# Optimization experiments

Hardware: AMD Instinct MI355X
Metric: run time of the kernel (lower is better)

The kernel has to match this reference:

```python
import jax, jax.numpy as jnp
import numpy as np

N_A, N_P = 50000, 100000          # author / paper node counts
E_W, E_C = 1600000, 3200000       # writes & written_by edges, cites edges
NEG_SLOPE = 0.2                   # DGL GATConv default leaky_relu slope
EPS = 1e-12                       # F.normalize eps


def _gat(h_src, h_dst, src, dst, W, al, ar, b, n_dst):
    """DGL GATConv: fc -> per-head additive attention -> edge softmax -> weighted sum + bias."""
    H, F = al.shape
    fs = (h_src @ W.T).reshape(-1, H, F)            # [Ns, H, F]
    fd = (h_dst @ W.T).reshape(-1, H, F)            # [Nd, H, F]
    el = (fs * al).sum(-1)                          # [Ns, H]
    er = (fd * ar).sum(-1)                          # [Nd, H]
    e = jax.nn.leaky_relu(el[src] + er[dst], NEG_SLOPE)      # [E, H]
    m = jax.lax.stop_gradient(jax.ops.segment_max(e, dst, num_segments=n_dst))
    ex = jnp.exp(e - m[dst])
    s = jax.ops.segment_sum(ex, dst, num_segments=n_dst)
    a = ex / s[dst]                                 # edge softmax per dst node, per head
    rst = jax.ops.segment_sum(fs[src] * a[:, :, None], dst, num_segments=n_dst)
    return rst + b.reshape(H, F)                    # [Nd, H, F]


def _l2norm(x):
    return x / jnp.maximum(jnp.linalg.norm(x, axis=1, keepdims=True), EPS)


def setup_inputs() -> dict:
    key = jax.random.key(0)
    ks = iter(jax.random.split(key, 64))
    def nrm(shape, scale=0.1):
        return jax.random.normal(next(ks), shape, dtype=jnp.float32) * scale
    inp = {
        'feat_author': jax.random.normal(next(ks), (N_A, 128), dtype=jnp.float32),
        'feat_paper':  jax.random.normal(next(ks), (N_P, 256), dtype=jnp.float32),
        'fm_W_author': nrm((64, 128)), 'fm_b_author': nrm((64,)),
        'fm_W_paper':  nrm((64, 256)), 'fm_b_paper':  nrm((64,)),
    }
    for e in ('writes', 'written_by', 'cites'):
        inp[f'g1_{e}_W'] = nrm((64, 64)); inp[f'g1_{e}_al'] = nrm((4, 16))
        inp[f'g1_{e}_ar'] = nrm((4, 16)); inp[f'g1_{e}_b'] = nrm((64,))
        inp[f'g2_{e}_W'] = nrm((64, 64)); inp[f'g2_{e}_al'] = nrm((1, 64))
        inp[f'g2_{e}_ar'] = nrm((1, 64)); inp[f'g2_{e}_b'] = nrm((64,))
    inp['w_src'] = jax.random.randint(next(ks), (E_W,), 0, N_A, dtype=jnp.int32)
    inp['w_dst'] = jax.random.randint(next(ks), (E_W,), 0, N_P, dtype=jnp.int32)
    inp['wb_src'] = jax.random.randint(next(ks), (E_W,), 0, N_P, dtype=jnp.int32)
    inp['wb_dst'] = jax.random.randint(next(ks), (E_W,), 0, N_A, dtype=jnp.int32)
    inp['c_src'] = jax.random.randint(next(ks), (E_C,), 0, N_P, dtype=jnp.int32)
    inp['c_dst'] = jax.random.randint(next(ks), (E_C,), 0, N_P, dtype=jnp.int32)
    return inp


def reference(feat_author, feat_paper, fm_W_author, fm_b_author, fm_W_paper, fm_b_paper,
              g1_writes_W, g1_writes_al, g1_writes_ar, g1_writes_b,
              g2_writes_W, g2_writes_al, g2_writes_ar, g2_writes_b,
              g1_written_by_W, g1_written_by_al, g1_written_by_ar, g1_written_by_b,
              g2_written_by_W, g2_written_by_al, g2_written_by_ar, g2_written_by_b,
              g1_cites_W, g1_cites_al, g1_cites_ar, g1_cites_b,
              g2_cites_W, g2_cites_al, g2_cites_ar, g2_cites_b,
              w_src, w_dst, wb_src, wb_dst, c_src, c_dst):
    # FeatureMappingLayer: per-ntype Linear -> relu, out_dim 64
    h_a = jax.nn.relu(feat_author @ fm_W_author.T + fm_b_author)
    h_p = jax.nn.relu(feat_paper @ fm_W_paper.T + fm_b_paper)
    # NodeAttentionLayer: per-etype GATConv(64 -> 16, 4 heads), flatten, sum over incoming etypes
    h1_p = (_gat(h_a, h_p, w_src, w_dst, g1_writes_W, g1_writes_al, g1_writes_ar, g1_writes_b, N_P)
            + _gat(h_p, h_p, c_src, c_dst, g1_cites_W, g1_cites_al, g1_cites_ar, g1_cites_b, N_P)
           ).reshape(N_P, 64)
    h1_a = _gat(h_p, h_a, wb_src, wb_dst, g1_written_by_W, g1_written_by_al, g1_written_by_ar,
                g1_written_by_b, N_A).reshape(N_A, 64)
    # gat2: per-etype GATConv(64 -> 64, 1 head) on h1[:, :64] (== h1), squeeze, sum
    h2_p = (_gat(h1_a, h1_p, w_src, w_dst, g2_writes_W, g2_writes_al, g2_writes_ar, g2_writes_b, N_P)
            + _gat(h1_p, h1_p, c_src, c_dst, g2_cites_W, g2_cites_al, g2_cites_ar, g2_cites_b, N_P)
           ).reshape(N_P, 64)
    h2_a = _gat(h1_p, h1_a, wb_src, wb_dst, g2_written_by_W, g2_written_by_al, g2_written_by_ar,
                g2_written_by_b, N_A).reshape(N_A, 64)
    # F.normalize(p=2, dim=1)
    return (_l2norm(h2_a), _l2norm(h2_p))
```

## Files before the change

kernel.cpp:

```cpp
#include <hip/hip_runtime.h>
#include <hip/hip_bf16.h>

#define N_A 50000
#define N_P 100000
#define E_W 1600000
#define E_C 3200000
#define HA (N_A*64)
#define HP (N_P*64)

typedef __attribute__((ext_vector_type(8))) short short8_t;
typedef __attribute__((ext_vector_type(4))) float f32x4;

__device__ __forceinline__ unsigned short f2b(float f)
{
    __hip_bfloat16 b = __float2bfloat16(f);
    return *reinterpret_cast<unsigned short*>(&b);
}

__global__ __launch_bounds__(256) void gemm_fm2(
        const float* __restrict__ X0, const float* __restrict__ W0,
        const float* __restrict__ b0, float* __restrict__ out0, int M0, int K0, int nb0,
        const float* __restrict__ X1, const float* __restrict__ W1,
        const float* __restrict__ b1, float* __restrict__ out1, int M1, int K1)
{
    __shared__ unsigned short Xs[128][72];
    __shared__ unsigned short Wsh[64][72];
    const float *X, *W, *bias; float* out; int M, K, row0;
    if ((int)blockIdx.x < nb0) {
        X = X0; W = W0; bias = b0; out = out0; M = M0; K = K0; row0 = blockIdx.x * 128;
    } else {
        X = X1; W = W1; bias = b1; out = out1; M = M1; K = K1;
        row0 = ((int)blockIdx.x - nb0) * 128;
    }
    int tid = threadIdx.x, lane = tid & 63, wv = tid >> 6;
    int m = lane & 15, kb = lane >> 4;

    f32x4 acc[2][4];
#pragma unroll
    for (int rb = 0; rb < 2; ++rb)
#pragma unroll
        for (int cb = 0; cb < 4; ++cb) acc[rb][cb] = (f32x4){0.f, 0.f, 0.f, 0.f};

    for (int k0 = 0; k0 < K; k0 += 64) {
        int rbase = (tid >> 4) * 8;
        int c4 = (tid & 15) * 4;
#pragma unroll
        for (int i = 0; i < 8; ++i) {
            int rg = row0 + rbase + i; if (rg >= M) rg = M - 1;
            float4 v = *reinterpret_cast<const float4*>(&X[(long)rg * K + k0 + c4]);
            Xs[rbase + i][c4 + 0] = f2b(v.x);
            Xs[rbase + i][c4 + 1] = f2b(v.y);
            Xs[rbase + i][c4 + 2] = f2b(v.z);
            Xs[rbase + i][c4 + 3] = f2b(v.w);
        }
        int wr = tid >> 2;
        int wc = (tid & 3) * 16;
#pragma unroll
        for (int q = 0; q < 4; ++q) {
            float4 v = *reinterpret_cast<const float4*>(&W[(long)wr * K + k0 + wc + q * 4]);
            Wsh[wr][wc + q * 4 + 0] = f2b(v.x);
            Wsh[wr][wc + q * 4 + 1] = f2b(v.y);
            Wsh[wr][wc + q * 4 + 2] = f2b(v.z);
            Wsh[wr][wc + q * 4 + 3] = f2b(v.w);
        }
        __syncthreads();
#pragma unroll
        for (int kc = 0; kc < 2; ++kc) {
            short8_t a0 = *reinterpret_cast<const short8_t*>(&Xs[wv * 32 + m][kc * 32 + kb * 8]);
            short8_t a1 = *reinterpret_cast<const short8_t*>(&Xs[wv * 32 + 16 + m][kc * 32 + kb * 8]);
#pragma unroll
            for (int cb = 0; cb < 4; ++cb) {
                short8_t b = *reinterpret_cast<const short8_t*>(&Wsh[cb * 16 + m][kc * 32 + kb * 8]);
                acc[0][cb] = __builtin_amdgcn_mfma_f32_16x16x32_bf16(a0, b, acc[0][cb], 0, 0, 0);
                acc[1][cb] = __builtin_amdgcn_mfma_f32_16x16x32_bf16(a1, b, acc[1][cb], 0, 0, 0);
            }
        }
        __syncthreads();
    }

#pragma unroll
    for (int rb = 0; rb < 2; ++rb)
#pragma unroll
    for (int j = 0; j < 4; ++j) {
        int r = row0 + wv * 32 + rb * 16 + (lane >> 4) * 4 + j;
        if (r < M) {
#pragma unroll
            for (int cb = 0; cb < 4; ++cb) {
                int c = cb * 16 + m;
                float v = acc[rb][cb][j] + bias[c];
                out[(long)r * 64 + c] = fmaxf(v, 0.f);
            }
        }
    }
}

__global__ __launch_bounds__(256) void proj3(
        const float* __restrict__ X0, const float* __restrict__ W0,
        unsigned short* __restrict__ o0, int M0, int nb0,
        const float* __restrict__ X1, const float* __restrict__ W1,
        unsigned short* __restrict__ o1, int M1, int nb1,
        const float* __restrict__ X2, const float* __restrict__ W2,
        unsigned short* __restrict__ o2, int M2)
{
    __shared__ unsigned short Xs[128][72];
    __shared__ unsigned short Wsh[64][72];
    const float *X, *W; unsigned short* out; int M, row0;
    if ((int)blockIdx.x < nb0) {
        X = X0; W = W0; out = o0; M = M0; row0 = blockIdx.x * 128;
    } else if ((int)blockIdx.x < nb0 + nb1) {
        X = X1; W = W1; out = o1; M = M1; row0 = ((int)blockIdx.x - nb0) * 128;
    } else {
        X = X2; W = W2; out = o2; M = M2; row0 = ((int)blockIdx.x - nb0 - nb1) * 128;
    }
    int tid = threadIdx.x, lane = tid & 63, wv = tid >> 6;
    int m = lane & 15, kb = lane >> 4;

    int rbase = (tid >> 4) * 8;
    int c4 = (tid & 15) * 4;
#pragma unroll
    for (int i = 0; i < 8; ++i) {
        int rg = row0 + rbase + i; if (rg >= M) rg = M - 1;
        float4 v = *reinterpret_cast<const float4*>(&X[(long)rg * 64 + c4]);
        Xs[rbase + i][c4 + 0] = f2b(v.x);
        Xs[rbase + i][c4 + 1] = f2b(v.y);
        Xs[rbase + i][c4 + 2] = f2b(v.z);
        Xs[rbase + i][c4 + 3] = f2b(v.w);
    }
    int wr = tid >> 2;
    int wc = (tid & 3) * 16;
#pragma unroll
    for (int q = 0; q < 4; ++q) {
        float4 v = *reinterpret_cast<const float4*>(&W[(long)wr * 64 + wc + q * 4]);
        Wsh[wr][wc + q * 4 + 0] = f2b(v.x);
        Wsh[wr][wc + q * 4 + 1] = f2b(v.y);
        Wsh[wr][wc + q * 4 + 2] = f2b(v.z);
        Wsh[wr][wc + q * 4 + 3] = f2b(v.w);
    }
    __syncthreads();

    f32x4 acc[2][4];
#pragma unroll
    for (int rb = 0; rb < 2; ++rb)
#pragma unroll
        for (int cb = 0; cb < 4; ++cb) acc[rb][cb] = (f32x4){0.f, 0.f, 0.f, 0.f};
#pragma unroll
    for (int kc = 0; kc < 2; ++kc) {
        short8_t a0 = *reinterpret_cast<const short8_t*>(&Xs[wv * 32 + m][kc * 32 + kb * 8]);
        short8_t a1 = *reinterpret_cast<const short8_t*>(&Xs[wv * 32 + 16 + m][kc * 32 + kb * 8]);
#pragma unroll
        for (int cb = 0; cb < 4; ++cb) {
            short8_t b = *reinterpret_cast<const short8_t*>(&Wsh[cb * 16 + m][kc * 32 + kb * 8]);
            acc[0][cb] = __builtin_amdgcn_mfma_f32_16x16x32_bf16(a0, b, acc[0][cb], 0, 0, 0);
            acc[1][cb] = __builtin_amdgcn_mfma_f32_16x16x32_bf16(a1, b, acc[1][cb], 0, 0, 0);
        }
    }
#pragma unroll
    for (int rb = 0; rb < 2; ++rb)
#pragma unroll
    for (int j = 0; j < 4; ++j) {
        int r = row0 + wv * 32 + rb * 16 + (lane >> 4) * 4 + j;
        if (r < M) {
#pragma unroll
            for (int cb = 0; cb < 4; ++cb)
                out[(long)r * 64 + cb * 16 + m] = f2b(acc[rb][cb][j]);
        }
    }
}

struct PA { const float* W; const float* a; float* o; int H; };
__global__ void prep_attn12(PA p0, PA p1, PA p2, PA p3, PA p4, PA p5,
                            PA p6, PA p7, PA p8, PA p9, PA p10, PA p11)
{
    PA p;
    switch (blockIdx.x) {
        case 0: p = p0; break;  case 1: p = p1; break;  case 2: p = p2; break;
        case 3: p = p3; break;  case 4: p = p4; break;  case 5: p = p5; break;
        case 6: p = p6; break;  case 7: p = p7; break;  case 8: p = p8; break;
        case 9: p = p9; break;  case 10: p = p10; break; default: p = p11; break;
    }
    int k = threadIdx.x;
    int F = 64 / p.H;
    for (int hh = 0; hh < p.H; ++hh) {
        float s = 0.f;
        for (int f = 0; f < F; ++f)
            s = fmaf(p.W[(hh * F + f) * 64 + k], p.a[hh * F + f], s);
        p.o[k * p.H + hh] = s;
    }
}

__global__ __launch_bounds__(256) void attnvec_mat(
        const float* __restrict__ hP, int NPn,
        const float* __restrict__ fP0, float* __restrict__ oP0,
        const float* __restrict__ fP1, float* __restrict__ oP1,
        const float* __restrict__ fP2, float* __restrict__ oP2,
        const float* __restrict__ fP3, float* __restrict__ oP3,
        const float* __restrict__ hA, int NAn,
        const float* __restrict__ fA0, float* __restrict__ oA0,
        const float* __restrict__ fA1, float* __restrict__ oA1,
        int H, int hb)
{
    __shared__ float hs[64 * 66];
    int tid = threadIdx.x;
    int slotsP = (H == 4) ? 16 : 4;
    int npbP = 256 / slotsP;
    int blocksP = (NPn + npbP - 1) / npbP;

    const float* hsrc; int node0, npb, slots, ncols, N;
    const float* fv0; const float* fv1; const float* fv2; const float* fv3;
    float* ov0; float* ov1; float* ov2; float* ov3;
    if ((int)blockIdx.x < blocksP) {
        hsrc = hP; N = NPn; slots = slotsP; npb = npbP;
        node0 = blockIdx.x * npb;
        ncols = 4 * H;
        fv0 = fP0; ov0 = oP0; fv1 = fP1; ov1 = oP1;
        fv2 = fP2; ov2 = oP2; fv3 = fP3; ov3 = oP3;
    } else {
        int b = (int)blockIdx.x - blocksP;
        hsrc = hA; N = NAn;
        slots = (H == 4) ? 8 : 4; npb = 256 / slots;
        node0 = b * npb;
        ncols = 2 * H;
        fv0 = fA0; ov0 = oA0; fv1 = fA1; ov1 = oA1;
        fv2 = fA0; ov2 = oA0; fv3 = fA1; ov3 = oA1;
    }

    for (int idx = tid; idx < npb * 64; idx += 256) {
        int row = idx >> 6, k = idx & 63;
        int g = node0 + row; if (g >= N) g = N - 1;
        hs[row * 66 + k] = hsrc[(long)g * 64 + k];
    }
    __syncthreads();

    int sshift = (slots == 16) ? 4 : (slots == 8) ? 3 : 2;
    int nl = tid >> sshift;
    int c = tid & (slots - 1);
    int node = node0 + nl;
    if (node >= N || c >= ncols || nl >= npb) return;
    int f = c >> hb;
    int hh = c & (H - 1);
    const float* fv = (f == 0) ? fv0 : (f == 1) ? fv1 : (f == 2) ? fv2 : fv3;
    float* ov = (f == 0) ? ov0 : (f == 1) ? ov1 : (f == 2) ? ov2 : ov3;

    float s = 0.f;
    const float* hrow = &hs[nl * 66];
#pragma unroll 8
    for (int k = 0; k < 64; ++k)
        s = fmaf(hrow[k], fv[k * H + hh], s);
    ov[(long)node * H + hh] = s;
}

__global__ void bucket_hist3(const int* __restrict__ d0, int E0, int* __restrict__ b0,
                             const int* __restrict__ d1, int E1, int* __restrict__ b1,
                             const int* __restrict__ d2, int E2, int* __restrict__ b2,
                             int shift, int blocksPer)
{
    int g = blockIdx.x / blocksPer, bb = blockIdx.x - g * blocksPer;
    const int* dst = g == 0 ? d0 : g == 1 ? d1 : d2;
    int E = g == 0 ? E0 : g == 1 ? E1 : E2;
    int* bcnt = g == 0 ? b0 : g == 1 ? b1 : b2;
    __shared__ int h[256];
    int tid = threadIdx.x;
    h[tid] = 0;
    __syncthreads();
    for (long i = (long)bb * 256 + tid; i < E; i += (long)blocksPer * 256)
        atomicAdd(&h[dst[i] >> shift], 1);
    __syncthreads();
    if (h[tid]) atomicAdd(&bcnt[tid], h[tid]);
}

__global__ void bucket_scan3(int* __restrict__ bcnt, int* __restrict__ bstart,
                             int* __restrict__ gcur,
                             int* __restrict__ o0, int Nn0, int Ee0,
                             int* __restrict__ o1, int Nn1, int Ee1,
                             int* __restrict__ o2, int Nn2, int Ee2)
{
    int g = blockIdx.x;
    int* bc = bcnt + g * 256;
    int* bs = bstart + g * 257;
    int* gc = gcur + g * 256;
    int* offs = g == 0 ? o0 : g == 1 ? o1 : o2;
    int N = g == 0 ? Nn0 : g == 1 ? Nn1 : Nn2;
    int E = g == 0 ? Ee0 : g == 1 ? Ee1 : Ee2;
    __shared__ int sc[256];
    int tid = threadIdx.x;
    int v = bc[tid];
    sc[tid] = v;
    __syncthreads();
    for (int off = 1; off < 256; off <<= 1) {
        int t = (tid >= off) ? sc[tid - off] : 0;
        __syncthreads();
        sc[tid] += t;
        __syncthreads();
    }
    int excl = sc[tid] - v;
    bs[tid] = excl;
    gc[tid] = excl;
    if (tid == 255) bs[256] = E;
    if (tid == 0) offs[N] = E;
}

#define EPT 8
__global__ __launch_bounds__(256) void part3(
        const int* __restrict__ s0, const int* __restrict__ d0, int E0, int nb0,
        uint2* __restrict__ p0,
        const int* __restrict__ s1, const int* __restrict__ d1, int E1, int nb1,
        uint2* __restrict__ p1,
        const int* __restrict__ s2g, const int* __restrict__ d2g, int E2,
        uint2* __restrict__ p2,
        int* __restrict__ gcur3, int shift)
{
    const int* src; const int* dst; int E; uint2* pairs; int* gcur; long base;
    if ((int)blockIdx.x < nb0) {
        src = s0; dst = d0; E = E0; pairs = p0; gcur = gcur3;
        base = (long)blockIdx.x * (256 * EPT);
    } else if ((int)blockIdx.x < nb0 + nb1) {
        src = s1; dst = d1; E = E1; pairs = p1; gcur = gcur3 + 256;
        base = (long)((int)blockIdx.x - nb0) * (256 * EPT);
    } else {
        src = s2g; dst = d2g; E = E2; pairs = p2; gcur = gcur3 + 512;
        base = (long)((int)blockIdx.x - nb0 - nb1) * (256 * EPT);
    }
    __shared__ int hcnt[256];
    __shared__ int hbase[256];
    int tid = threadIdx.x;
    hcnt[tid] = 0;
    __syncthreads();
    int b[EPT], r[EPT], s[EPT], d[EPT];
#pragma unroll
    for (int k = 0; k < EPT; ++k) {
        long idx = base + k * 256 + tid;
        if (idx < E) {
            s[k] = src[idx]; d[k] = dst[idx];
            b[k] = d[k] >> shift;
            r[k] = atomicAdd(&hcnt[b[k]], 1);
        } else b[k] = -1;
    }
    __syncthreads();
    if (hcnt[tid]) hbase[tid] = atomicAdd(&gcur[tid], hcnt[tid]);
    __syncthreads();
#pragma unroll
    for (int k = 0; k < EPT; ++k) {
        if (b[k] >= 0)
            pairs[hbase[b[k]] + r[k]] = make_uint2((unsigned)s[k], (unsigned)d[k]);
    }
}

__global__ __launch_bounds__(512) void csr_fin3(
        const uint2* __restrict__ p0, const int* __restrict__ bs0,
        int* __restrict__ of0, int* __restrict__ c0, int N0, int NB0,
        const uint2* __restrict__ p1, const int* __restrict__ bs1,
        int* __restrict__ of1, int* __restrict__ c1, int N1, int NB1,
        const uint2* __restrict__ p2, const int* __restrict__ bs2,
        int* __restrict__ of2, int* __restrict__ c2, int N2,
        int shift)
{
    const uint2* pairs; const int* bstart; int* offs; int* csr; int N, b;
    if ((int)blockIdx.x < NB0) {
        pairs = p0; bstart = bs0; offs = of0; csr = c0; N = N0; b = blockIdx.x;
    } else if ((int)blockIdx.x < NB0 + NB1) {
        pairs = p1; bstart = bs1; offs = of1; csr = c1; N = N1; b = (int)blockIdx.x - NB0;
    } else {
        pairs = p2; bstart = bs2; offs = of2; csr = c2; N = N2;
        b = (int)blockIdx.x - NB0 - NB1;
    }
    __shared__ int cnt[512];
    __shared__ int sc[512];
    int tid = threadIdx.x;
    int d0 = b << shift;
    int pS = bstart[b], pE = bstart[b + 1];
    cnt[tid] = 0;
    __syncthreads();
    for (int i = pS + tid; i < pE; i += 512)
        atomicAdd(&cnt[pairs[i].y - d0], 1);
    __syncthreads();
    int v = cnt[tid];
    sc[tid] = v;
    __syncthreads();
    for (int off = 1; off < 512; off <<= 1) {
        int t = (tid >= off) ? sc[tid - off] : 0;
        __syncthreads();
        sc[tid] += t;
        __syncthreads();
    }
    int excl = sc[tid] - v;
    if (d0 + tid < N) offs[d0 + tid] = pS + excl;
    cnt[tid] = excl;
    __syncthreads();
    for (int i = pS + tid; i < pE; i += 512) {
        uint2 u = pairs[i];
        int p = atomicAdd(&cnt[u.y - d0], 1);
        csr[pS + p] = (int)u.x;
    }
}

__device__ __forceinline__ void gat_graph(int d, const int* __restrict__ offs,
        const int* __restrict__ csr, const float* __restrict__ el,
        const float* __restrict__ er, const unsigned short* __restrict__ P,
        int hshift, int lane, float* o)
{
    int H = 1 << hshift;
    int off = offs[d];
    int n = offs[d + 1] - off;
    if (n == 0) return;
    int g8 = lane >> 3;
    int fo = (lane & 7) * 8;
    int hf = (hshift == 2) ? ((lane & 7) >> 1) : 0;
    int h = lane & (H - 1);
    float erd = er[d * H + h];
    int estep = 64 >> hshift;
    int i0 = lane >> hshift;
    float acc[8];
#pragma unroll
    for (int q = 0; q < 8; ++q) acc[q] = 0.f;
    float ssum = 0.f;

    int sn_c = 0; float elv_c = 0.f;
    if (i0 < n) { sn_c = csr[off + i0]; elv_c = el[sn_c * H + h]; }

    for (int base = 0; base < n; base += estep) {
        int inext = base + estep + i0;
        int sn_n = 0; float elv_n = 0.f;
        if (inext < n) { sn_n = csr[off + inext]; elv_n = el[sn_n * H + h]; }

        float a = 0.f;
        if (base + i0 < n) {
            float v = elv_c + erd;
            v = v > 0.f ? v : 0.2f * v;
            a = __expf(v);
            ssum += a;
        }
        int rounds = min(estep, n - base);
#pragma unroll 2
        for (int r = 0; r * 8 < rounds; ++r) {
            int sl = r * 8 + g8;
            int lsn = sl << hshift;
            int s2 = __shfl(sn_c, lsn, 64);
            float a2 = __shfl(a, lsn | hf, 64);
            uint4 u = *reinterpret_cast<const uint4*>(&P[(long)s2 * 64 + fo]);
            acc[0] = fmaf(__uint_as_float(u.x << 16), a2, acc[0]);
            acc[1] = fmaf(__uint_as_float(u.x & 0xffff0000u), a2, acc[1]);
            acc[2] = fmaf(__uint_as_float(u.y << 16), a2, acc[2]);
            acc[3] = fmaf(__uint_as_float(u.y & 0xffff0000u), a2, acc[3]);
            acc[4] = fmaf(__uint_as_float(u.z << 16), a2, acc[4]);
            acc[5] = fmaf(__uint_as_float(u.z & 0xffff0000u), a2, acc[5]);
            acc[6] = fmaf(__uint_as_float(u.w << 16), a2, acc[6]);
            acc[7] = fmaf(__uint_as_float(u.w & 0xffff0000u), a2, acc[7]);
        }
        sn_c = sn_n; elv_c = elv_n;
    }

    for (int oo = H; oo < 64; oo <<= 1) ssum += __shfl_xor(ssum, oo, 64);
    float rinv = 1.f / __shfl(ssum, hf, 64);
#pragma unroll
    for (int q = 0; q < 8; ++q) {
        acc[q] += __shfl_xor(acc[q], 8, 64);
        acc[q] += __shfl_xor(acc[q], 16, 64);
        acc[q] += __shfl_xor(acc[q], 32, 64);
        o[q] = fmaf(acc[q], rinv, o[q]);
    }
}

__global__ void gat_fused(
        int NPn, const int* __restrict__ w_offs, const int* __restrict__ w_csr,
        const float* __restrict__ el_w, const float* __restrict__ er_w,
        const unsigned short* __restrict__ Pw,
        const int* __restrict__ c_offs, const int* __restrict__ c_csr,
        const float* __restrict__ el_c, const float* __restrict__ er_c,
        const unsigned short* __restrict__ Pc,
        const float* __restrict__ bP0, const float* __restrict__ bP1,
        float* __restrict__ outP,
        int NAn, const int* __restrict__ wb_offs, const int* __restrict__ wb_csr,
        const float* __restrict__ el_wb, const float* __restrict__ er_wb,
        const unsigned short* __restrict__ Pwb,
        const float* __restrict__ bA0, float* __restrict__ outA,
        int hshift, int doNorm)
{
    int blocksP = (NPn + 3) >> 2;
    int lane = threadIdx.x & 63;
    int sub = threadIdx.x >> 6;
    int fo = (lane & 7) * 8;
    float o[8];
    float* dst;

    if ((int)blockIdx.x < blocksP) {
        int d = ((int)blockIdx.x << 2) | sub;
        if (d >= NPn) return;
#pragma unroll
        for (int q = 0; q < 8; ++q) o[q] = bP0[fo + q] + bP1[fo + q];
        gat_graph(d, w_offs, w_csr, el_w, er_w, Pw, hshift, lane, o);
        gat_graph(d, c_offs, c_csr, el_c, er_c, Pc, hshift, lane, o);
        dst = outP + (long)d * 64;
    } else {
        int d = (((int)blockIdx.x - blocksP) << 2) | sub;
        if (d >= NAn) return;
#pragma unroll
        for (int q = 0; q < 8; ++q) o[q] = bA0[fo + q];
        gat_graph(d, wb_offs, wb_csr, el_wb, er_wb, Pwb, hshift, lane, o);
        dst = outA + (long)d * 64;
    }

    if (doNorm) {
        float ss = 0.f;
#pragma unroll
        for (int q = 0; q < 8; ++q) ss = fmaf(o[q], o[q], ss);
        ss += __shfl_xor(ss, 1, 64);
        ss += __shfl_xor(ss, 2, 64);
        ss += __shfl_xor(ss, 4, 64);
        float sc = 1.f / fmaxf(sqrtf(ss), 1e-12f);
#pragma unroll
        for (int q = 0; q < 8; ++q) o[q] *= sc;
    }
    if (lane < 8) {
        float4 o0, o1;
        o0.x = o[0]; o0.y = o[1]; o0.z = o[2]; o0.w = o[3];
        o1.x = o[4]; o1.y = o[5]; o1.z = o[6]; o1.w = o[7];
        *reinterpret_cast<float4*>(dst + fo) = o0;
        *reinterpret_cast<float4*>(dst + fo + 4) = o1;
    }
}

extern "C" void kernel_launch(void* const* d_in, const int* in_sizes, int n_in,
                              void* d_out, int out_size, void* d_ws, size_t ws_size,
                              hipStream_t stream)
{
    const float* feat_a = (const float*)d_in[0];
    const float* feat_p = (const float*)d_in[1];
    const float* fmWa = (const float*)d_in[2];
    const float* fmba = (const float*)d_in[3];
    const float* fmWp = (const float*)d_in[4];
    const float* fmbp = (const float*)d_in[5];
    const float* g1w_W = (const float*)d_in[6];  const float* g1w_al = (const float*)d_in[7];
    const float* g1w_ar = (const float*)d_in[8]; const float* g1w_b = (const float*)d_in[9];
    const float* g2w_W = (const float*)d_in[10]; const float* g2w_al = (const float*)d_in[11];
    const float* g2w_ar = (const float*)d_in[12]; const float* g2w_b = (const float*)d_in[13];
    const float* g1wb_W = (const float*)d_in[14]; const float* g1wb_al = (const float*)d_in[15];
    const float* g1wb_ar = (const float*)d_in[16]; const float* g1wb_b = (const float*)d_in[17];
    const float* g2wb_W = (const float*)d_in[18]; const float* g2wb_al = (const float*)d_in[19];
    const float* g2wb_ar = (const float*)d_in[20]; const float* g2wb_b = (const float*)d_in[21];
    const float* g1c_W = (const float*)d_in[22]; const float* g1c_al = (const float*)d_in[23];
    const float* g1c_ar = (const float*)d_in[24]; const float* g1c_b = (const float*)d_in[25];
    const float* g2c_W = (const float*)d_in[26]; const float* g2c_al = (const float*)d_in[27];
    const float* g2c_ar = (const float*)d_in[28]; const float* g2c_b = (const float*)d_in[29];
    const int* w_src = (const int*)d_in[30];
    const int* w_dst = (const int*)d_in[31];
    const int* wb_src = (const int*)d_in[32];
    const int* wb_dst = (const int*)d_in[33];
    const int* c_src = (const int*)d_in[34];
    const int* c_dst = (const int*)d_in[35];

    float* ws = (float*)d_ws;
    size_t off = 0;
    auto alloc = [&](size_t n) { float* p = ws + off; off += n; return p; };
    float* h_a  = alloc(HA);
    float* h_p  = alloc(HP);
    float* h1_p = alloc(HP);
    float* h1_a = alloc(HA);
    uint2* pairs_w  = (uint2*)h_a;
    uint2* pairs_c  = (uint2*)h_a + E_W;
    uint2* pairs_wb = (uint2*)h_a + E_W + E_C;
    unsigned short* Pw  = (unsigned short*)alloc(HA / 2 + 16);
    unsigned short* Pc  = (unsigned short*)alloc(HP / 2 + 16);
    unsigned short* Pwb = (unsigned short*)alloc(HP / 2 + 16);
    float* el_w  = alloc((size_t)N_A * 4);
    float* er_w  = alloc((size_t)N_P * 4);
    float* el_c  = alloc((size_t)N_P * 4);
    float* er_c  = alloc((size_t)N_P * 4);
    float* el_wb = alloc((size_t)N_P * 4);
    float* er_wb = alloc((size_t)N_A * 4);
    float* fold  = alloc(12 * 256);
    int* w_offs  = (int*)alloc(N_P + 1);
    int* c_offs  = (int*)alloc(N_P + 1);
    int* wb_offs = (int*)alloc(N_A + 1);
    int* bcnt3   = (int*)alloc(3 * 256);
    int* bstart3 = (int*)alloc(3 * 257);
    int* gcur3   = (int*)alloc(3 * 256);
    int* w_csr   = (int*)alloc(E_W);
    int* c_csr   = (int*)alloc(E_C);
    int* wb_csr  = (int*)alloc(E_W);

    float* wal_w1 = fold + 0*256,  *war_w1 = fold + 1*256;
    float* wal_c1 = fold + 2*256,  *war_c1 = fold + 3*256;
    float* wal_b1 = fold + 4*256,  *war_b1 = fold + 5*256;
    float* wal_w2 = fold + 6*256,  *war_w2 = fold + 7*256;
    float* wal_c2 = fold + 8*256,  *war_c2 = fold + 9*256;
    float* wal_b2 = fold + 10*256, *war_b2 = fold + 11*256;

    const int SHIFT = 9;
    int NB_P = (N_P + 511) >> 9;
    int NB_A = (N_A + 511) >> 9;

    hipMemsetAsync(bcnt3, 0, 3 * 256 * sizeof(int), stream);
    bucket_hist3<<<3 * 256, 256, 0, stream>>>(w_dst, E_W, bcnt3,
                                              c_dst, E_C, bcnt3 + 256,
                                              wb_dst, E_W, bcnt3 + 512, SHIFT, 256);
    bucket_scan3<<<3, 256, 0, stream>>>(bcnt3, bstart3, gcur3,
                                        w_offs, N_P, E_W,
                                        c_offs, N_P, E_C,
                                        wb_offs, N_A, E_W);
    {
        int nbW = (E_W + 2047) / 2048, nbC = (E_C + 2047) / 2048;
        part3<<<nbW + nbC + nbW, 256, 0, stream>>>(
            w_src, w_dst, E_W, nbW, pairs_w,
            c_src, c_dst, E_C, nbC, pairs_c,
            wb_src, wb_dst, E_W, pairs_wb, gcur3, SHIFT);
        csr_fin3<<<NB_P + NB_P + NB_A, 512, 0, stream>>>(
            pairs_w, bstart3, w_offs, w_csr, N_P, NB_P,
            pairs_c, bstart3 + 257, c_offs, c_csr, N_P, NB_P,
            pairs_wb, bstart3 + 514, wb_offs, wb_csr, N_A, SHIFT);
    }

    prep_attn12<<<12, 64, 0, stream>>>(
        PA{g1w_W,  g1w_al,  wal_w1, 4}, PA{g1w_W,  g1w_ar,  war_w1, 4},
        PA{g1c_W,  g1c_al,  wal_c1, 4}, PA{g1c_W,  g1c_ar,  war_c1, 4},
        PA{g1wb_W, g1wb_al, wal_b1, 4}, PA{g1wb_W, g1wb_ar, war_b1, 4},
        PA{g2w_W,  g2w_al,  wal_w2, 1}, PA{g2w_W,  g2w_ar,  war_w2, 1},
        PA{g2c_W,  g2c_al,  wal_c2, 1}, PA{g2c_W,  g2c_ar,  war_c2, 1},
        PA{g2wb_W, g2wb_al, wal_b2, 1}, PA{g2wb_W, g2wb_ar, war_b2, 1});

    {
        int nb0 = (N_A + 127) / 128;
        int nb1 = (N_P + 127) / 128;
        gemm_fm2<<<nb0 + nb1, 256, 0, stream>>>(feat_a, fmWa, fmba, h_a, N_A, 128, nb0,
                                                feat_p, fmWp, fmbp, h_p, N_P, 256);
    }

    int nbA = (N_A + 127) / 128, nbP = (N_P + 127) / 128;
    int gatGrid = (N_P + 3) / 4 + (N_A + 3) / 4;

    {
        int npbP = 16, npbA = 32;
        int grid = (N_P + npbP - 1) / npbP + (N_A + npbA - 1) / npbA;
        attnvec_mat<<<grid, 256, 0, stream>>>(
            h_p, N_P, wal_c1, el_c, war_c1, er_c, war_w1, er_w, wal_b1, el_wb,
            h_a, N_A, wal_w1, el_w, war_b1, er_wb, 4, 2);
    }
    proj3<<<nbA + 2 * nbP, 256, 0, stream>>>(h_a, g1w_W, Pw, N_A, nbA,
                                             h_p, g1c_W, Pc, N_P, nbP,
                                             h_p, g1wb_W, Pwb, N_P);
    gat_fused<<<gatGrid, 256, 0, stream>>>(
        N_P, w_offs, w_csr, el_w, er_w, Pw,
        c_offs, c_csr, el_c, er_c, Pc, g1w_b, g1c_b, h1_p,
        N_A, wb_offs, wb_csr, el_wb, er_wb, Pwb, g1wb_b, h1_a, 2, 0);

    {
        int npbP = 64, npbA = 64;
        int grid = (N_P + npbP - 1) / npbP + (N_A + npbA - 1) / npbA;
        attnvec_mat<<<grid, 256, 0, stream>>>(
            h1_p, N_P, wal_c2, el_c, war_c2, er_c, war_w2, er_w, wal_b2, el_wb,
            h1_a, N_A, wal_w2, el_w, war_b2, er_wb, 1, 0);
    }
    proj3<<<nbA + 2 * nbP, 256, 0, stream>>>(h1_a, g2w_W, Pw, N_A, nbA,
                                             h1_p, g2c_W, Pc, N_P, nbP,
                                             h1_p, g2wb_W, Pwb, N_P);
    float* out = (float*)d_out;
    gat_fused<<<gatGrid, 256, 0, stream>>>(
        N_P, w_offs, w_csr, el_w, er_w, Pw,
        c_offs, c_csr, el_c, er_c, Pc, g2w_b, g2c_b, out + HA,
        N_A, wb_offs, wb_csr, el_wb, er_wb, Pwb, g2wb_b, out, 0, 1);
}
```

Before: 735.4 us.

## Fuse attention-logit computation into projection kernel and use nontemporal CSR loads

Removes the separate attnvec_mat kernel and computes the el/er attention logits inside the projection kernel, reusing the bf16 node rows already staged in shared memory. This saves one launch per layer and a second full read of the hidden features. The logits are now computed from bf16-rounded inputs rather than fp32, which slightly changes precision. The CSR index loads in the GAT aggregation are also made nontemporal to reduce cache pollution.

```diff
diff --git a/kernel.cpp b/kernel.cpp
--- a/kernel.cpp
+++ b/kernel.cpp
@@ -15,6 +15,10 @@
 {
     __hip_bfloat16 b = __float2bfloat16(f);
     return *reinterpret_cast<unsigned short*>(&b);
+}
+__device__ __forceinline__ float b2f(unsigned short u)
+{
+    return __uint_as_float((unsigned)u << 16);
 }
 
 __global__ __launch_bounds__(256) void gemm_fm2(
@@ -94,23 +98,35 @@
     }
 }
 
-__global__ __launch_bounds__(256) void proj3(
+__global__ __launch_bounds__(256) void proj3a(
         const float* __restrict__ X0, const float* __restrict__ W0,
         unsigned short* __restrict__ o0, int M0, int nb0,
+        const float* __restrict__ fA0, float* __restrict__ eA0,
+        const float* __restrict__ fA1, float* __restrict__ eA1,
         const float* __restrict__ X1, const float* __restrict__ W1,
         unsigned short* __restrict__ o1, int M1, int nb1,
+        const float* __restrict__ fP0, float* __restrict__ eP0,
+        const float* __restrict__ fP1, float* __restrict__ eP1,
+        const float* __restrict__ fP2, float* __restrict__ eP2,
+        const float* __restrict__ fP3, float* __restrict__ eP3,
         const float* __restrict__ X2, const float* __restrict__ W2,
-        unsigned short* __restrict__ o2, int M2)
+        unsigned short* __restrict__ o2, int M2, int H)
 {
     __shared__ unsigned short Xs[128][72];
     __shared__ unsigned short Wsh[64][72];
-    const float *X, *W; unsigned short* out; int M, row0;
+    const float *X, *W; unsigned short* out; int M, row0, nf;
+    const float* fv[4]; float* ev[4];
     if ((int)blockIdx.x < nb0) {
         X = X0; W = W0; out = o0; M = M0; row0 = blockIdx.x * 128;
+        nf = 2; fv[0] = fA0; ev[0] = eA0; fv[1] = fA1; ev[1] = eA1;
+        fv[2] = fA0; ev[2] = eA0; fv[3] = fA1; ev[3] = eA1;
     } else if ((int)blockIdx.x < nb0 + nb1) {
         X = X1; W = W1; out = o1; M = M1; row0 = ((int)blockIdx.x - nb0) * 128;
+        nf = 4; fv[0] = fP0; ev[0] = eP0; fv[1] = fP1; ev[1] = eP1;
+        fv[2] = fP2; ev[2] = eP2; fv[3] = fP3; ev[3] = eP3;
     } else {
         X = X2; W = W2; out = o2; M = M2; row0 = ((int)blockIdx.x - nb0 - nb1) * 128;
+        nf = 0;
     }
     int tid = threadIdx.x, lane = tid & 63, wv = tid >> 6;
     int m = lane & 15, kb = lane >> 4;
@@ -165,6 +181,25 @@
                 out[(long)r * 64 + cb * 16 + m] = f2b(acc[rb][cb][j]);
         }
     }
+
+    if (nf) {
+        int tot = 128 * nf * H;
+        for (int t = tid; t < tot; t += 256) {
+            int row = t / (nf * H);
+            int rest = t - row * (nf * H);
+            int f = rest / H;
+            int hh = rest - f * H;
+            int r = row0 + row;
+            if (r >= M) continue;
+            const unsigned short* xr = Xs[row];
+            const float* fvv = fv[f];
+            float s = 0.f;
+#pragma unroll 8
+            for (int k = 0; k < 64; ++k)
+                s = fmaf(b2f(xr[k]), fvv[k * H + hh], s);
+            ev[f][(long)r * H + hh] = s;
+        }
+    }
 }
 
 struct PA { const float* W; const float* a; float* o; int H; };
@@ -186,67 +221,6 @@
             s = fmaf(p.W[(hh * F + f) * 64 + k], p.a[hh * F + f], s);
         p.o[k * p.H + hh] = s;
     }
-}
-
-__global__ __launch_bounds__(256) void attnvec_mat(
-        const float* __restrict__ hP, int NPn,
-        const float* __restrict__ fP0, float* __restrict__ oP0,
-        const float* __restrict__ fP1, float* __restrict__ oP1,
-        const float* __restrict__ fP2, float* __restrict__ oP2,
-        const float* __restrict__ fP3, float* __restrict__ oP3,
-        const float* __restrict__ hA, int NAn,
-        const float* __restrict__ fA0, float* __restrict__ oA0,
-        const float* __restrict__ fA1, float* __restrict__ oA1,
-        int H, int hb)
-{
-    __shared__ float hs[64 * 66];
-    int tid = threadIdx.x;
-    int slotsP = (H == 4) ? 16 : 4;
-    int npbP = 256 / slotsP;
-    int blocksP = (NPn + npbP - 1) / npbP;
-
-    const float* hsrc; int node0, npb, slots, ncols, N;
-    const float* fv0; const float* fv1; const float* fv2; const float* fv3;
-    float* ov0; float* ov1; float* ov2; float* ov3;
-    if ((int)blockIdx.x < blocksP) {
-        hsrc = hP; N = NPn; slots = slotsP; npb = npbP;
-        node0 = blockIdx.x * npb;
-        ncols = 4 * H;
-        fv0 = fP0; ov0 = oP0; fv1 = fP1; ov1 = oP1;
-        fv2 = fP2; ov2 = oP2; fv3 = fP3; ov3 = oP3;
-    } else {
-        int b = (int)blockIdx.x - blocksP;
-        hsrc = hA; N = NAn;
-        slots = (H == 4) ? 8 : 4; npb = 256 / slots;
-        node0 = b * npb;
-        ncols = 2 * H;
-        fv0 = fA0; ov0 = oA0; fv1 = fA1; ov1 = oA1;
-        fv2 = fA0; ov2 = oA0; fv3 = fA1; ov3 = oA1;
-    }
-
-    for (int idx = tid; idx < npb * 64; idx += 256) {
-        int row = idx >> 6, k = idx & 63;
-        int g = node0 + row; if (g >= N) g = N - 1;
-        hs[row * 66 + k] = hsrc[(long)g * 64 + k];
-    }
-    __syncthreads();
-
-    int sshift = (slots == 16) ? 4 : (slots == 8) ? 3 : 2;
-    int nl = tid >> sshift;
-    int c = tid & (slots - 1);
-    int node = node0 + nl;
-    if (node >= N || c >= ncols || nl >= npb) return;
-    int f = c >> hb;
-    int hh = c & (H - 1);
-    const float* fv = (f == 0) ? fv0 : (f == 1) ? fv1 : (f == 2) ? fv2 : fv3;
-    float* ov = (f == 0) ? ov0 : (f == 1) ? ov1 : (f == 2) ? ov2 : ov3;
-
-    float s = 0.f;
-    const float* hrow = &hs[nl * 66];
-#pragma unroll 8
-    for (int k = 0; k < 64; ++k)
-        s = fmaf(hrow[k], fv[k * H + hh], s);
-    ov[(long)node * H + hh] = s;
 }
 
 __global__ void bucket_hist3(const int* __restrict__ d0, int E0, int* __restrict__ b0,
@@ -415,12 +389,12 @@
     float ssum = 0.f;
 
     int sn_c = 0; float elv_c = 0.f;
-    if (i0 < n) { sn_c = csr[off + i0]; elv_c = el[sn_c * H + h]; }
+    if (i0 < n) { sn_c = __builtin_nontemporal_load(&csr[off + i0]); elv_c = el[sn_c * H + h]; }
 
     for (int base = 0; base < n; base += estep) {
         int inext = base + estep + i0;
         int sn_n = 0; float elv_n = 0.f;
-        if (inext < n) { sn_n = csr[off + inext]; elv_n = el[sn_n * H + h]; }
+        if (inext < n) { sn_n = __builtin_nontemporal_load(&csr[off + inext]); elv_n = el[sn_n * H + h]; }
 
         float a = 0.f;
         if (base + i0 < n) {
@@ -627,31 +601,19 @@
     int nbA = (N_A + 127) / 128, nbP = (N_P + 127) / 128;
     int gatGrid = (N_P + 3) / 4 + (N_A + 3) / 4;
 
-    {
-        int npbP = 16, npbA = 32;
-        int grid = (N_P + npbP - 1) / npbP + (N_A + npbA - 1) / npbA;
-        attnvec_mat<<<grid, 256, 0, stream>>>(
-            h_p, N_P, wal_c1, el_c, war_c1, er_c, war_w1, er_w, wal_b1, el_wb,
-            h_a, N_A, wal_w1, el_w, war_b1, er_wb, 4, 2);
-    }
-    proj3<<<nbA + 2 * nbP, 256, 0, stream>>>(h_a, g1w_W, Pw, N_A, nbA,
-                                             h_p, g1c_W, Pc, N_P, nbP,
-                                             h_p, g1wb_W, Pwb, N_P);
+    proj3a<<<nbA + 2 * nbP, 256, 0, stream>>>(
+        h_a, g1w_W, Pw, N_A, nbA, wal_w1, el_w, war_b1, er_wb,
+        h_p, g1c_W, Pc, N_P, nbP, wal_c1, el_c, war_c1, er_c, war_w1, er_w, wal_b1, el_wb,
+        h_p, g1wb_W, Pwb, N_P, 4);
     gat_fused<<<gatGrid, 256, 0, stream>>>(
         N_P, w_offs, w_csr, el_w, er_w, Pw,
         c_offs, c_csr, el_c, er_c, Pc, g1w_b, g1c_b, h1_p,
         N_A, wb_offs, wb_csr, el_wb, er_wb, Pwb, g1wb_b, h1_a, 2, 0);
 
-    {
-        int npbP = 64, npbA = 64;
-        int grid = (N_P + npbP - 1) / npbP + (N_A + npbA - 1) / npbA;
-        attnvec_mat<<<grid, 256, 0, stream>>>(
-            h1_p, N_P, wal_c2, el_c, war_c2, er_c, war_w2, er_w, wal_b2, el_wb,
-            h1_a, N_A, wal_w2, el_w, war_b2, er_wb, 1, 0);
-    }
-    proj3<<<nbA + 2 * nbP, 256, 0, stream>>>(h1_a, g2w_W, Pw, N_A, nbA,
-                                             h1_p, g2c_W, Pc, N_P, nbP,
-                                             h1_p, g2wb_W, Pwb, N_P);
+    proj3a<<<nbA + 2 * nbP, 256, 0, stream>>>(
+        h1_a, g2w_W, Pw, N_A, nbA, wal_w2, el_w, war_b2, er_wb,
+        h1_p, g2c_W, Pc, N_P, nbP, wal_c2, el_c, war_c2, er_c, war_w2, er_w, wal_b2, el_wb,
+        h1_p, g2wb_W, Pwb, N_P, 1);
     float* out = (float*)d_out;
     gat_fused<<<gatGrid, 256, 0, stream>>>(
         N_P, w_offs, w_csr, el_w, er_w, Pw,
```

Result: no change. 734.7 us (-0.1%).
